# Kernel tuning notes

Measured on AMD Instinct MI355X. Metric: run time of the kernel, lower is better.

The kernel has to match this reference:

```python
import jax, jax.numpy as jnp
import numpy as np

N = 8192
IN_F = 512
OUT_F = 128
NEG_BIG = -9.0e15


def setup_inputs() -> dict:
    key = jax.random.key(0)
    k_x, k_adj, k_w, k_a1, k_a2 = jax.random.split(key, 5)
    X = jax.random.normal(k_x, (N, IN_F), dtype=jnp.float32)
    adj = jax.random.randint(k_adj, (N, N), 0, 2, dtype=jnp.int32)
    # xavier_uniform with gain=1.414
    gain = 1.414
    lim_w = gain * np.sqrt(6.0 / (IN_F + OUT_F))
    W = jax.random.uniform(k_w, (IN_F, OUT_F), minval=-lim_w, maxval=lim_w, dtype=jnp.float32)
    lim_a = gain * np.sqrt(6.0 / (OUT_F + 1))
    a_1 = jax.random.uniform(k_a1, (OUT_F, 1), minval=-lim_a, maxval=lim_a, dtype=jnp.float32)
    a_2 = jax.random.uniform(k_a2, (OUT_F, 1), minval=-lim_a, maxval=lim_a, dtype=jnp.float32)
    return {"X": X, "adj": adj, "W": W, "a_1": a_1, "a_2": a_2}


def reference(X, adj, W, a_1, a_2):
    h = X @ W                         # [N, out]
    Wh1 = h @ a_1                     # [N, 1]
    Wh2 = h @ a_2                     # [N, 1]
    alpha = Wh1 + Wh2.T               # [N, N] broadcast score sum
    s = jax.nn.sigmoid(alpha)
    masked = jnp.where(adj > 0, s, jnp.float32(NEG_BIG))
    attn = jax.nn.softmax(masked, axis=1)  # dropout p=0.0 -> identity
    return attn @ h                   # [N, out]
```

## Files before the change

kernel.cpp:

```cpp
#include <hip/hip_runtime.h>
#include <hip/hip_bf16.h>

#define N_NODES 8192
#define IN_F 512
#define OUT_F 128
#define KSHIFT 4
#define KP (1 << KSHIFT)
#define KT_PER (256 >> KSHIFT)
#define LOG2E 1.4426950408889634f

typedef unsigned short u16;
typedef unsigned int u32;
typedef short s16x8 __attribute__((ext_vector_type(8)));
typedef float f32x4 __attribute__((ext_vector_type(4)));
typedef u32 u32x4 __attribute__((ext_vector_type(4)));
typedef int i32x4 __attribute__((ext_vector_type(4)));

__device__ __forceinline__ u16 f2bf(float f) {
    union { float f; unsigned u; } x; x.f = f;
    unsigned r = x.u + 0x7FFFu + ((x.u >> 16) & 1u);
    return (u16)(r >> 16);
}

__device__ __forceinline__ u32 packbf2(float a, float b) {
    __hip_bfloat162 h = __float22bfloat162_rn(make_float2(a, b));
    u32 u; __builtin_memcpy(&u, &h, 4);
    return u;
}

__device__ __forceinline__ float edge_p(float wh1, float w2, int keep) {
    float alpha = wh1 + w2;
    float e = exp2f(-LOG2E * alpha);
    float s = __builtin_amdgcn_rcpf(1.0f + e);
    float p = exp2f(LOG2E * s);
    return keep ? p : 0.0f;
}

__global__ void repack_W(const float* __restrict__ W, u16* __restrict__ W_frag) {
    int tid = blockIdx.x * 256 + threadIdx.x;
    int j = tid & 7;
    int lane = (tid >> 3) & 63;
    int nt = (tid >> 9) & 7;
    int kt = tid >> 12;
    int k = kt * 32 + (lane >> 4) * 8 + j;
    int n = nt * 16 + (lane & 15);
    W_frag[tid] = f2bf(W[k * OUT_F + n]);
}

__global__ void compute_Wa(const float* __restrict__ W, const float* __restrict__ a1,
                           const float* __restrict__ a2,
                           float* __restrict__ Wa1, float* __restrict__ Wa2) {
    int k = blockIdx.x * 256 + threadIdx.x;
    if (k >= IN_F) return;
    float s1 = 0.f, s2 = 0.f;
    #pragma unroll 8
    for (int n = 0; n < OUT_F; n++) {
        float w = W[k * OUT_F + n];
        s1 += w * a1[n];
        s2 += w * a2[n];
    }
    Wa1[k] = s1; Wa2[k] = s2;
}

__global__ __launch_bounds__(256)
void gemm_h(const float* __restrict__ X, const u16* __restrict__ W_frag,
            const float* __restrict__ Wa1, const float* __restrict__ Wa2,
            float* __restrict__ Wh1, float* __restrict__ Wh2,
            u16* __restrict__ h_frag) {
    int tid = threadIdx.x;
    int wave = tid >> 6;
    int lane = tid & 63;
    int quad = lane >> 4;
    int lid = lane & 15;
    int rbase = blockIdx.x * 64 + wave * 16;
    const float* xrow = X + (size_t)(rbase + lid) * IN_F;
    const s16x8* Wf = (const s16x8*)W_frag;
    f32x4 acc[8] = {};
    float p1 = 0.f, p2 = 0.f;

    for (int kt = 0; kt < 16; kt++) {
        int k0 = kt * 32 + quad * 8;
        float4 x0 = *(const float4*)(xrow + k0);
        float4 x1 = *(const float4*)(xrow + k0 + 4);
        u32x4 uv;
        uv.x = packbf2(x0.x, x0.y); uv.y = packbf2(x0.z, x0.w);
        uv.z = packbf2(x1.x, x1.y); uv.w = packbf2(x1.z, x1.w);
        s16x8 a = __builtin_bit_cast(s16x8, uv);
        float4 wa = *(const float4*)(Wa1 + k0);
        float4 wb = *(const float4*)(Wa1 + k0 + 4);
        float4 wc = *(const float4*)(Wa2 + k0);
        float4 wd = *(const float4*)(Wa2 + k0 + 4);
        p1 += x0.x*wa.x + x0.y*wa.y + x0.z*wa.z + x0.w*wa.w
            + x1.x*wb.x + x1.y*wb.y + x1.z*wb.z + x1.w*wb.w;
        p2 += x0.x*wc.x + x0.y*wc.y + x0.z*wc.z + x0.w*wc.w
            + x1.x*wd.x + x1.y*wd.y + x1.z*wd.z + x1.w*wd.w;
        #pragma unroll
        for (int nt = 0; nt < 8; nt++) {
            s16x8 b = Wf[(kt * 8 + nt) * 64 + lane];
            acc[nt] = __builtin_amdgcn_mfma_f32_16x16x32_bf16(a, b, acc[nt], 0, 0, 0);
        }
    }

    #pragma unroll
    for (int reg = 0; reg < 4; reg++) {
        int row = rbase + quad * 4 + reg;
        int ktile = row >> 5, kl = row & 31;
        int lane2 = (kl >> 3) * 16 + lid, j2 = kl & 7;
        #pragma unroll
        for (int nt = 0; nt < 8; nt++)
            h_frag[(size_t)((ktile * 8 + nt) * 64 + lane2) * 8 + j2] = f2bf(acc[nt][reg]);
    }
    p1 += __shfl_xor(p1, 16, 64); p1 += __shfl_xor(p1, 32, 64);
    p2 += __shfl_xor(p2, 16, 64); p2 += __shfl_xor(p2, 32, 64);
    if (lane < 16) { Wh1[rbase + lid] = p1; Wh2[rbase + lid] = p2; }
}

__global__ __launch_bounds__(256)
void attn_kernel(const int* __restrict__ adj, const float* __restrict__ Wh1,
                 const float* __restrict__ Wh2, const u16* __restrict__ h_frag,
                 float* __restrict__ out_part, float* __restrict__ sum_part) {
    int tid = threadIdx.x;
    int wave = tid >> 6;
    int lane = tid & 63;
    int quad = lane >> 4;
    int lid = lane & 15;
    int rtile = blockIdx.x >> KSHIFT;
    int kh = blockIdx.x & (KP - 1);
    int rbase = rtile * 128 + wave * 32;
    int r0 = rbase + lid, r1 = r0 + 16;

    float wh10 = Wh1[r0], wh11 = Wh1[r1];
    f32x4 acc0[8] = {}, acc1[8] = {};
    float ps0 = 0.f, ps1 = 0.f;
    const s16x8* Hf = (const s16x8*)h_frag;
    const i32x4* adjrow0 = (const i32x4*)(adj + (size_t)r0 * N_NODES);
    const i32x4* adjrow1 = (const i32x4*)(adj + (size_t)r1 * N_NODES);

    const int kt0 = kh * KT_PER;
    #pragma unroll 4
    for (int kt = kt0; kt < kt0 + KT_PER; kt++) {
        int k0 = kt * 32 + quad * 8;
        int q4 = k0 >> 2;
        i32x4 aj0a = __builtin_nontemporal_load(adjrow0 + q4);
        i32x4 aj0b = __builtin_nontemporal_load(adjrow0 + q4 + 1);
        i32x4 aj1a = __builtin_nontemporal_load(adjrow1 + q4);
        i32x4 aj1b = __builtin_nontemporal_load(adjrow1 + q4 + 1);
        float4 w20 = *(const float4*)(Wh2 + k0);
        float4 w21 = *(const float4*)(Wh2 + k0 + 4);

        float e0 = edge_p(wh10, w20.x, aj0a.x), e1 = edge_p(wh10, w20.y, aj0a.y);
        float e2 = edge_p(wh10, w20.z, aj0a.z), e3 = edge_p(wh10, w20.w, aj0a.w);
        float e4 = edge_p(wh10, w21.x, aj0b.x), e5 = edge_p(wh10, w21.y, aj0b.y);
        float e6 = edge_p(wh10, w21.z, aj0b.z), e7 = edge_p(wh10, w21.w, aj0b.w);
        ps0 += ((e0 + e1) + (e2 + e3)) + ((e4 + e5) + (e6 + e7));
        u32x4 uv0;
        uv0.x = packbf2(e0, e1); uv0.y = packbf2(e2, e3);
        uv0.z = packbf2(e4, e5); uv0.w = packbf2(e6, e7);

        float f0 = edge_p(wh11, w20.x, aj1a.x), f1 = edge_p(wh11, w20.y, aj1a.y);
        float f2 = edge_p(wh11, w20.z, aj1a.z), f3 = edge_p(wh11, w20.w, aj1a.w);
        float f4 = edge_p(wh11, w21.x, aj1b.x), f5 = edge_p(wh11, w21.y, aj1b.y);
        float f6 = edge_p(wh11, w21.z, aj1b.z), f7 = edge_p(wh11, w21.w, aj1b.w);
        ps1 += ((f0 + f1) + (f2 + f3)) + ((f4 + f5) + (f6 + f7));
        u32x4 uv1;
        uv1.x = packbf2(f0, f1); uv1.y = packbf2(f2, f3);
        uv1.z = packbf2(f4, f5); uv1.w = packbf2(f6, f7);

        s16x8 af0 = __builtin_bit_cast(s16x8, uv0);
        s16x8 af1 = __builtin_bit_cast(s16x8, uv1);

        #pragma unroll
        for (int nt = 0; nt < 8; nt++) {
            s16x8 b = Hf[(kt * 8 + nt) * 64 + lane];
            acc0[nt] = __builtin_amdgcn_mfma_f32_16x16x32_bf16(af0, b, acc0[nt], 0, 0, 0);
            acc1[nt] = __builtin_amdgcn_mfma_f32_16x16x32_bf16(af1, b, acc1[nt], 0, 0, 0);
        }
    }

    ps0 += __shfl_xor(ps0, 16, 64); ps0 += __shfl_xor(ps0, 32, 64);
    ps1 += __shfl_xor(ps1, 16, 64); ps1 += __shfl_xor(ps1, 32, 64);
    if (quad == 0) {
        sum_part[(size_t)kh * N_NODES + r0] = ps0;
        sum_part[(size_t)kh * N_NODES + r1] = ps1;
    }

    #pragma unroll
    for (int nt = 0; nt < 8; nt++) {
        #pragma unroll
        for (int reg = 0; reg < 4; reg++) {
            int row0 = rbase + quad * 4 + reg;
            int col = nt * 16 + lid;
            out_part[((size_t)kh * N_NODES + row0) * OUT_F + col] = acc0[nt][reg];
            out_part[((size_t)kh * N_NODES + row0 + 16) * OUT_F + col] = acc1[nt][reg];
        }
    }
}

__global__ void finalize(const float* __restrict__ out_part,
                         const float* __restrict__ sum_part,
                         float* __restrict__ out) {
    int gid = blockIdx.x * 256 + threadIdx.x;
    int i = gid >> 7;
    float s = 0.f, v = 0.f;
    #pragma unroll
    for (int kh = 0; kh < KP; kh++) {
        s += sum_part[(size_t)kh * N_NODES + i];
        v += out_part[(size_t)kh * N_NODES * OUT_F + gid];
    }
    out[gid] = v / s;
}

extern "C" void kernel_launch(void* const* d_in, const int* in_sizes, int n_in,
                              void* d_out, int out_size, void* d_ws, size_t ws_size,
                              hipStream_t stream) {
    const float* X   = (const float*)d_in[0];
    const int*   adj = (const int*)d_in[1];
    const float* W   = (const float*)d_in[2];
    const float* a1  = (const float*)d_in[3];
    const float* a2  = (const float*)d_in[4];

    const size_t BASE = (size_t)4 << 20;
    char* ws = (char*)d_ws;
    float* Wh1 = (float*)(ws);
    float* Wh2 = (float*)(ws + (32 << 10));
    float* Wa1 = (float*)(ws + (64 << 10));
    float* Wa2 = (float*)(ws + (66 << 10));
    u16* W_frag = (u16*)(ws + (128 << 10));
    u16* h_frag = (u16*)(ws + (256 << 10));
    float* out_part = (float*)(ws + BASE);
    float* sum_part = (float*)(ws + BASE + ((size_t)KP << 22));
    float* out = (float*)d_out;

    hipLaunchKernelGGL(repack_W, dim3(256), dim3(256), 0, stream, W, W_frag);
    hipLaunchKernelGGL(compute_Wa, dim3(2), dim3(256), 0, stream, W, a1, a2, Wa1, Wa2);
    hipLaunchKernelGGL(gemm_h, dim3(128), dim3(256), 0, stream,
                       X, W_frag, Wa1, Wa2, Wh1, Wh2, h_frag);
    hipLaunchKernelGGL(attn_kernel, dim3(64 << KSHIFT), dim3(256), 0, stream,
                       adj, Wh1, Wh2, h_frag, out_part, sum_part);
    hipLaunchKernelGGL(finalize, dim3((N_NODES * OUT_F) / 256), dim3(256), 0, stream,
                       out_part, sum_part, out);
}
```

Measured before the change: 509.2 us.

## Load adjacency rows coalesced, ballot into bitmasks via LDS; split gemm_h across waves

The attention kernel now reads each adjacency row as contiguous 256-column chunks across the whole wave. It compresses the rows to 64-bit ballot masks held in shared memory, and each lane pulls its keep bits from there. This replaces the old strided per-lane 32-byte row loads. The split factor drops from 16 to 8, which halves partial-output traffic. gemm_h now spreads column tiles across waves with 16 rows per block and 4x more blocks. Only wave 0 computes Wh1/Wh2. The shared-memory handoff has no barrier, but each wave touches only its own slot, so it relies on intra-wave ordering.

```diff
diff --git a/kernel.cpp b/kernel.cpp
--- a/kernel.cpp
+++ b/kernel.cpp
@@ -4,13 +4,15 @@
 #define N_NODES 8192
 #define IN_F 512
 #define OUT_F 128
-#define KSHIFT 4
+#define KSHIFT 3
 #define KP (1 << KSHIFT)
-#define KT_PER (256 >> KSHIFT)
+#define COLS_PER (N_NODES / KP)
+#define NCHUNK (COLS_PER / 256)
 #define LOG2E 1.4426950408889634f
 
 typedef unsigned short u16;
 typedef unsigned int u32;
+typedef unsigned long long u64;
 typedef short s16x8 __attribute__((ext_vector_type(8)));
 typedef float f32x4 __attribute__((ext_vector_type(4)));
 typedef u32 u32x4 __attribute__((ext_vector_type(4)));
@@ -72,11 +74,12 @@
     int lane = tid & 63;
     int quad = lane >> 4;
     int lid = lane & 15;
-    int rbase = blockIdx.x * 64 + wave * 16;
+    int rbase = blockIdx.x * 16;
     const float* xrow = X + (size_t)(rbase + lid) * IN_F;
     const s16x8* Wf = (const s16x8*)W_frag;
-    f32x4 acc[8] = {};
+    f32x4 acc0 = {}, acc1 = {};
     float p1 = 0.f, p2 = 0.f;
+    int nt0 = wave * 2;
 
     for (int kt = 0; kt < 16; kt++) {
         int k0 = kt * 32 + quad * 8;
@@ -86,19 +89,20 @@
         uv.x = packbf2(x0.x, x0.y); uv.y = packbf2(x0.z, x0.w);
         uv.z = packbf2(x1.x, x1.y); uv.w = packbf2(x1.z, x1.w);
         s16x8 a = __builtin_bit_cast(s16x8, uv);
-        float4 wa = *(const float4*)(Wa1 + k0);
-        float4 wb = *(const float4*)(Wa1 + k0 + 4);
-        float4 wc = *(const float4*)(Wa2 + k0);
-        float4 wd = *(const float4*)(Wa2 + k0 + 4);
-        p1 += x0.x*wa.x + x0.y*wa.y + x0.z*wa.z + x0.w*wa.w
-            + x1.x*wb.x + x1.y*wb.y + x1.z*wb.z + x1.w*wb.w;
-        p2 += x0.x*wc.x + x0.y*wc.y + x0.z*wc.z + x0.w*wc.w
-            + x1.x*wd.x + x1.y*wd.y + x1.z*wd.z + x1.w*wd.w;
-        #pragma unroll
-        for (int nt = 0; nt < 8; nt++) {
-            s16x8 b = Wf[(kt * 8 + nt) * 64 + lane];
-            acc[nt] = __builtin_amdgcn_mfma_f32_16x16x32_bf16(a, b, acc[nt], 0, 0, 0);
-        }
+        if (wave == 0) {
+            float4 wa = *(const float4*)(Wa1 + k0);
+            float4 wb = *(const float4*)(Wa1 + k0 + 4);
+            float4 wc = *(const float4*)(Wa2 + k0);
+            float4 wd = *(const float4*)(Wa2 + k0 + 4);
+            p1 += x0.x*wa.x + x0.y*wa.y + x0.z*wa.z + x0.w*wa.w
+                + x1.x*wb.x + x1.y*wb.y + x1.z*wb.z + x1.w*wb.w;
+            p2 += x0.x*wc.x + x0.y*wc.y + x0.z*wc.z + x0.w*wc.w
+                + x1.x*wd.x + x1.y*wd.y + x1.z*wd.z + x1.w*wd.w;
+        }
+        s16x8 b0 = Wf[(kt * 8 + nt0) * 64 + lane];
+        s16x8 b1 = Wf[(kt * 8 + nt0 + 1) * 64 + lane];
+        acc0 = __builtin_amdgcn_mfma_f32_16x16x32_bf16(a, b0, acc0, 0, 0, 0);
+        acc1 = __builtin_amdgcn_mfma_f32_16x16x32_bf16(a, b1, acc1, 0, 0, 0);
     }
 
     #pragma unroll
@@ -106,19 +110,22 @@
         int row = rbase + quad * 4 + reg;
         int ktile = row >> 5, kl = row & 31;
         int lane2 = (kl >> 3) * 16 + lid, j2 = kl & 7;
-        #pragma unroll
-        for (int nt = 0; nt < 8; nt++)
-            h_frag[(size_t)((ktile * 8 + nt) * 64 + lane2) * 8 + j2] = f2bf(acc[nt][reg]);
-    }
-    p1 += __shfl_xor(p1, 16, 64); p1 += __shfl_xor(p1, 32, 64);
-    p2 += __shfl_xor(p2, 16, 64); p2 += __shfl_xor(p2, 32, 64);
-    if (lane < 16) { Wh1[rbase + lid] = p1; Wh2[rbase + lid] = p2; }
+        h_frag[(size_t)((ktile * 8 + nt0) * 64 + lane2) * 8 + j2] = f2bf(acc0[reg]);
+        h_frag[(size_t)((ktile * 8 + nt0 + 1) * 64 + lane2) * 8 + j2] = f2bf(acc1[reg]);
+    }
+    if (wave == 0) {
+        p1 += __shfl_xor(p1, 16, 64); p1 += __shfl_xor(p1, 32, 64);
+        p2 += __shfl_xor(p2, 16, 64); p2 += __shfl_xor(p2, 32, 64);
+        if (lane < 16) { Wh1[rbase + lid] = p1; Wh2[rbase + lid] = p2; }
+    }
 }
 
 __global__ __launch_bounds__(256)
 void attn_kernel(const int* __restrict__ adj, const float* __restrict__ Wh1,
                  const float* __restrict__ Wh2, const u16* __restrict__ h_frag,
                  float* __restrict__ out_part, float* __restrict__ sum_part) {
+    __shared__ u64 lds_bits[4][2][32][4];
+
     int tid = threadIdx.x;
     int wave = tid >> 6;
     int lane = tid & 63;
@@ -133,47 +140,67 @@
     f32x4 acc0[8] = {}, acc1[8] = {};
     float ps0 = 0.f, ps1 = 0.f;
     const s16x8* Hf = (const s16x8*)h_frag;
-    const i32x4* adjrow0 = (const i32x4*)(adj + (size_t)r0 * N_NODES);
-    const i32x4* adjrow1 = (const i32x4*)(adj + (size_t)r1 * N_NODES);
-
-    const int kt0 = kh * KT_PER;
-    #pragma unroll 4
-    for (int kt = kt0; kt < kt0 + KT_PER; kt++) {
-        int k0 = kt * 32 + quad * 8;
-        int q4 = k0 >> 2;
-        i32x4 aj0a = __builtin_nontemporal_load(adjrow0 + q4);
-        i32x4 aj0b = __builtin_nontemporal_load(adjrow0 + q4 + 1);
-        i32x4 aj1a = __builtin_nontemporal_load(adjrow1 + q4);
-        i32x4 aj1b = __builtin_nontemporal_load(adjrow1 + q4 + 1);
-        float4 w20 = *(const float4*)(Wh2 + k0);
-        float4 w21 = *(const float4*)(Wh2 + k0 + 4);
-
-        float e0 = edge_p(wh10, w20.x, aj0a.x), e1 = edge_p(wh10, w20.y, aj0a.y);
-        float e2 = edge_p(wh10, w20.z, aj0a.z), e3 = edge_p(wh10, w20.w, aj0a.w);
-        float e4 = edge_p(wh10, w21.x, aj0b.x), e5 = edge_p(wh10, w21.y, aj0b.y);
-        float e6 = edge_p(wh10, w21.z, aj0b.z), e7 = edge_p(wh10, w21.w, aj0b.w);
-        ps0 += ((e0 + e1) + (e2 + e3)) + ((e4 + e5) + (e6 + e7));
-        u32x4 uv0;
-        uv0.x = packbf2(e0, e1); uv0.y = packbf2(e2, e3);
-        uv0.z = packbf2(e4, e5); uv0.w = packbf2(e6, e7);
-
-        float f0 = edge_p(wh11, w20.x, aj1a.x), f1 = edge_p(wh11, w20.y, aj1a.y);
-        float f2 = edge_p(wh11, w20.z, aj1a.z), f3 = edge_p(wh11, w20.w, aj1a.w);
-        float f4 = edge_p(wh11, w21.x, aj1b.x), f5 = edge_p(wh11, w21.y, aj1b.y);
-        float f6 = edge_p(wh11, w21.z, aj1b.z), f7 = edge_p(wh11, w21.w, aj1b.w);
-        ps1 += ((f0 + f1) + (f2 + f3)) + ((f4 + f5) + (f6 + f7));
-        u32x4 uv1;
-        uv1.x = packbf2(f0, f1); uv1.y = packbf2(f2, f3);
-        uv1.z = packbf2(f4, f5); uv1.w = packbf2(f6, f7);
-
-        s16x8 af0 = __builtin_bit_cast(s16x8, uv0);
-        s16x8 af1 = __builtin_bit_cast(s16x8, uv1);
-
+
+    for (int chunk = 0; chunk < NCHUNK; chunk++) {
+        int buf = chunk & 1;
+        int colbase = kh * COLS_PER + chunk * 256;
+
+        #pragma unroll 4
+        for (int r = 0; r < 32; r++) {
+            const i32x4* p = (const i32x4*)(adj + (size_t)(rbase + r) * N_NODES + colbase);
+            i32x4 v = p[lane];
+            u64 b0 = __ballot(v.x > 0);
+            u64 b1 = __ballot(v.y > 0);
+            u64 b2 = __ballot(v.z > 0);
+            u64 b3 = __ballot(v.w > 0);
+            if (lane == 0) {
+                lds_bits[wave][buf][r][0] = b0;
+                lds_bits[wave][buf][r][1] = b1;
+                lds_bits[wave][buf][r][2] = b2;
+                lds_bits[wave][buf][r][3] = b3;
+            }
+        }
+
+        u64 Ba[4], Bb[4];
         #pragma unroll
-        for (int nt = 0; nt < 8; nt++) {
-            s16x8 b = Hf[(kt * 8 + nt) * 64 + lane];
-            acc0[nt] = __builtin_amdgcn_mfma_f32_16x16x32_bf16(af0, b, acc0[nt], 0, 0, 0);
-            acc1[nt] = __builtin_amdgcn_mfma_f32_16x16x32_bf16(af1, b, acc1[nt], 0, 0, 0);
+        for (int j = 0; j < 4; j++) {
+            Ba[j] = lds_bits[wave][buf][lid][j];
+            Bb[j] = lds_bits[wave][buf][lid + 16][j];
+        }
+
+        #pragma unroll
+        for (int ktl = 0; ktl < 8; ktl++) {
+            int sh = ktl * 8 + quad * 2;
+            int col0 = colbase + ktl * 32 + quad * 8;
+            int ktg = (colbase >> 5) + ktl;
+            float4 w20 = *(const float4*)(Wh2 + col0);
+            float4 w21 = *(const float4*)(Wh2 + col0 + 4);
+            float w2v[8] = {w20.x, w20.y, w20.z, w20.w, w21.x, w21.y, w21.z, w21.w};
+
+            float ev[8], fv[8];
+            #pragma unroll
+            for (int j2 = 0; j2 < 8; j2++) {
+                int ka = (int)((Ba[j2 & 3] >> (sh + (j2 >> 2))) & 1ull);
+                int kb = (int)((Bb[j2 & 3] >> (sh + (j2 >> 2))) & 1ull);
+                ev[j2] = edge_p(wh10, w2v[j2], ka);
+                fv[j2] = edge_p(wh11, w2v[j2], kb);
+            }
+            ps0 += ((ev[0] + ev[1]) + (ev[2] + ev[3])) + ((ev[4] + ev[5]) + (ev[6] + ev[7]));
+            ps1 += ((fv[0] + fv[1]) + (fv[2] + fv[3])) + ((fv[4] + fv[5]) + (fv[6] + fv[7]));
+            u32x4 uv0, uv1;
+            uv0.x = packbf2(ev[0], ev[1]); uv0.y = packbf2(ev[2], ev[3]);
+            uv0.z = packbf2(ev[4], ev[5]); uv0.w = packbf2(ev[6], ev[7]);
+            uv1.x = packbf2(fv[0], fv[1]); uv1.y = packbf2(fv[2], fv[3]);
+            uv1.z = packbf2(fv[4], fv[5]); uv1.w = packbf2(fv[6], fv[7]);
+            s16x8 af0 = __builtin_bit_cast(s16x8, uv0);
+            s16x8 af1 = __builtin_bit_cast(s16x8, uv1);
+
+            #pragma unroll
+            for (int nt = 0; nt < 8; nt++) {
+                s16x8 b = Hf[(ktg * 8 + nt) * 64 + lane];
+                acc0[nt] = __builtin_amdgcn_mfma_f32_16x16x32_bf16(af0, b, acc0[nt], 0, 0, 0);
+                acc1[nt] = __builtin_amdgcn_mfma_f32_16x16x32_bf16(af1, b, acc1[nt], 0, 0, 0);
+            }
         }
     }
 
@@ -233,9 +260,9 @@
 
     hipLaunchKernelGGL(repack_W, dim3(256), dim3(256), 0, stream, W, W_frag);
     hipLaunchKernelGGL(compute_Wa, dim3(2), dim3(256), 0, stream, W, a1, a2, Wa1, Wa2);
-    hipLaunchKernelGGL(gemm_h, dim3(128), dim3(256), 0, stream,
+    hipLaunchKernelGGL(gemm_h, dim3(512), dim3(256), 0, stream,
                        X, W_frag, Wa1, Wa2, Wh1, Wh2, h_frag);
-    hipLaunchKernelGGL(attn_kernel, dim3(64 << KSHIFT), dim3(256), 0, stream,
+    hipLaunchKernelGGL(attn_kernel, dim3(64 * KP), dim3(256), 0, stream,
                        adj, Wh1, Wh2, h_frag, out_part, sum_part);
     hipLaunchKernelGGL(finalize, dim3((N_NODES * OUT_F) / 256), dim3(256), 0, stream,
                        out_part, sum_part, out);
```

Result: slower. 562.0 us (+10.4%).

## Split gemm_h across waves by column tiles and halve attention K-split

Applied to the files above, without the earlier changes.

gemm_h now assigns one 16-row tile per block, with each wave computing two of the eight output column tiles. This quadruples the grid to 512 blocks for better occupancy, and only wave 0 computes the Wh1/Wh2 projections. The attention kernel's K-split drops from 16 to 8 partitions, which halves partial-output traffic and finalize work but gives fewer, longer blocks. The adjacency loads also change from nontemporal to plain int4 loads, and the main loop unroll goes from 4 to 1, which may reduce latency hiding.

```diff
diff --git a/kernel.cpp b/kernel.cpp
--- a/kernel.cpp
+++ b/kernel.cpp
@@ -4,7 +4,7 @@
 #define N_NODES 8192
 #define IN_F 512
 #define OUT_F 128
-#define KSHIFT 4
+#define KSHIFT 3
 #define KP (1 << KSHIFT)
 #define KT_PER (256 >> KSHIFT)
 #define LOG2E 1.4426950408889634f
@@ -14,7 +14,6 @@
 typedef short s16x8 __attribute__((ext_vector_type(8)));
 typedef float f32x4 __attribute__((ext_vector_type(4)));
 typedef u32 u32x4 __attribute__((ext_vector_type(4)));
-typedef int i32x4 __attribute__((ext_vector_type(4)));
 
 __device__ __forceinline__ u16 f2bf(float f) {
     union { float f; unsigned u; } x; x.f = f;
@@ -72,11 +71,12 @@
     int lane = tid & 63;
     int quad = lane >> 4;
     int lid = lane & 15;
-    int rbase = blockIdx.x * 64 + wave * 16;
+    int rbase = blockIdx.x * 16;
     const float* xrow = X + (size_t)(rbase + lid) * IN_F;
     const s16x8* Wf = (const s16x8*)W_frag;
-    f32x4 acc[8] = {};
+    f32x4 acc0 = {}, acc1 = {};
     float p1 = 0.f, p2 = 0.f;
+    int nt0 = wave * 2;
 
     for (int kt = 0; kt < 16; kt++) {
         int k0 = kt * 32 + quad * 8;
@@ -86,19 +86,20 @@
         uv.x = packbf2(x0.x, x0.y); uv.y = packbf2(x0.z, x0.w);
         uv.z = packbf2(x1.x, x1.y); uv.w = packbf2(x1.z, x1.w);
         s16x8 a = __builtin_bit_cast(s16x8, uv);
-        float4 wa = *(const float4*)(Wa1 + k0);
-        float4 wb = *(const float4*)(Wa1 + k0 + 4);
-        float4 wc = *(const float4*)(Wa2 + k0);
-        float4 wd = *(const float4*)(Wa2 + k0 + 4);
+        if (wave == 0) {
+            float4 wa = *(const float4*)(Wa1 + k0);
+            float4 wb = *(const float4*)(Wa1 + k0 + 4);
+            float4 wc = *(const float4*)(Wa2 + k0);
+            float4 wd = *(const float4*)(Wa2 + k0 + 4);
         p1 += x0.x*wa.x + x0.y*wa.y + x0.z*wa.z + x0.w*wa.w
             + x1.x*wb.x + x1.y*wb.y + x1.z*wb.z + x1.w*wb.w;
         p2 += x0.x*wc.x + x0.y*wc.y + x0.z*wc.z + x0.w*wc.w
             + x1.x*wd.x + x1.y*wd.y + x1.z*wd.z + x1.w*wd.w;
-        #pragma unroll
-        for (int nt = 0; nt < 8; nt++) {
-            s16x8 b = Wf[(kt * 8 + nt) * 64 + lane];
-            acc[nt] = __builtin_amdgcn_mfma_f32_16x16x32_bf16(a, b, acc[nt], 0, 0, 0);
         }
+        s16x8 b0 = Wf[(kt * 8 + nt0) * 64 + lane];
+        s16x8 b1 = Wf[(kt * 8 + nt0 + 1) * 64 + lane];
+        acc0 = __builtin_amdgcn_mfma_f32_16x16x32_bf16(a, b0, acc0, 0, 0, 0);
+        acc1 = __builtin_amdgcn_mfma_f32_16x16x32_bf16(a, b1, acc1, 0, 0, 0);
     }
 
     #pragma unroll
@@ -106,13 +107,14 @@
         int row = rbase + quad * 4 + reg;
         int ktile = row >> 5, kl = row & 31;
         int lane2 = (kl >> 3) * 16 + lid, j2 = kl & 7;
-        #pragma unroll
-        for (int nt = 0; nt < 8; nt++)
-            h_frag[(size_t)((ktile * 8 + nt) * 64 + lane2) * 8 + j2] = f2bf(acc[nt][reg]);
-    }
-    p1 += __shfl_xor(p1, 16, 64); p1 += __shfl_xor(p1, 32, 64);
-    p2 += __shfl_xor(p2, 16, 64); p2 += __shfl_xor(p2, 32, 64);
-    if (lane < 16) { Wh1[rbase + lid] = p1; Wh2[rbase + lid] = p2; }
+        h_frag[(size_t)((ktile * 8 + nt0) * 64 + lane2) * 8 + j2] = f2bf(acc0[reg]);
+        h_frag[(size_t)((ktile * 8 + nt0 + 1) * 64 + lane2) * 8 + j2] = f2bf(acc1[reg]);
+    }
+    if (wave == 0) {
+        p1 += __shfl_xor(p1, 16, 64); p1 += __shfl_xor(p1, 32, 64);
+        p2 += __shfl_xor(p2, 16, 64); p2 += __shfl_xor(p2, 32, 64);
+        if (lane < 16) { Wh1[rbase + lid] = p1; Wh2[rbase + lid] = p2; }
+    }
 }
 
 __global__ __launch_bounds__(256)
@@ -133,18 +135,17 @@
     f32x4 acc0[8] = {}, acc1[8] = {};
     float ps0 = 0.f, ps1 = 0.f;
     const s16x8* Hf = (const s16x8*)h_frag;
-    const i32x4* adjrow0 = (const i32x4*)(adj + (size_t)r0 * N_NODES);
-    const i32x4* adjrow1 = (const i32x4*)(adj + (size_t)r1 * N_NODES);
+    const int* adjrow0 = adj + (size_t)r0 * N_NODES;
+    const int* adjrow1 = adj + (size_t)r1 * N_NODES;
 
     const int kt0 = kh * KT_PER;
-    #pragma unroll 4
+    #pragma unroll 1
     for (int kt = kt0; kt < kt0 + KT_PER; kt++) {
         int k0 = kt * 32 + quad * 8;
-        int q4 = k0 >> 2;
-        i32x4 aj0a = __builtin_nontemporal_load(adjrow0 + q4);
-        i32x4 aj0b = __builtin_nontemporal_load(adjrow0 + q4 + 1);
-        i32x4 aj1a = __builtin_nontemporal_load(adjrow1 + q4);
-        i32x4 aj1b = __builtin_nontemporal_load(adjrow1 + q4 + 1);
+        int4 aj0a = *(const int4*)(adjrow0 + k0);
+        int4 aj0b = *(const int4*)(adjrow0 + k0 + 4);
+        int4 aj1a = *(const int4*)(adjrow1 + k0);
+        int4 aj1b = *(const int4*)(adjrow1 + k0 + 4);
         float4 w20 = *(const float4*)(Wh2 + k0);
         float4 w21 = *(const float4*)(Wh2 + k0 + 4);
 
@@ -202,7 +203,6 @@
     int gid = blockIdx.x * 256 + threadIdx.x;
     int i = gid >> 7;
     float s = 0.f, v = 0.f;
-    #pragma unroll
     for (int kh = 0; kh < KP; kh++) {
         s += sum_part[(size_t)kh * N_NODES + i];
         v += out_part[(size_t)kh * N_NODES * OUT_F + gid];
@@ -233,9 +233,9 @@
 
     hipLaunchKernelGGL(repack_W, dim3(256), dim3(256), 0, stream, W, W_frag);
     hipLaunchKernelGGL(compute_Wa, dim3(2), dim3(256), 0, stream, W, a1, a2, Wa1, Wa2);
-    hipLaunchKernelGGL(gemm_h, dim3(128), dim3(256), 0, stream,
+    hipLaunchKernelGGL(gemm_h, dim3(512), dim3(256), 0, stream,
                        X, W_frag, Wa1, Wa2, Wh1, Wh2, h_frag);
-    hipLaunchKernelGGL(attn_kernel, dim3(64 << KSHIFT), dim3(256), 0, stream,
+    hipLaunchKernelGGL(attn_kernel, dim3(64 * KP), dim3(256), 0, stream,
                        adj, Wh1, Wh2, h_frag, out_part, sum_part);
     hipLaunchKernelGGL(finalize, dim3((N_NODES * OUT_F) / 256), dim3(256), 0, stream,
                        out_part, sum_part, out);
```

After: 438.0 us. 14.0% less time.
